# Optimization experiments

Hardware: AMD Instinct MI355X
Metric: run time of the kernel (lower is better)

Reference implementation:

```python
import jax, jax.numpy as jnp
import numpy as np

N = 50000   # nodes
E = 800000  # edges
D_FEAT = 128
D_HID = 128
D_EMB = 128


def _xavier(key, shape):
    fan_in, fan_out = shape
    lim = float(np.sqrt(6.0 / (fan_in + fan_out)))
    return jax.random.uniform(key, shape, jnp.float32, -lim, lim)


def setup_inputs() -> dict:
    key = jax.random.key(0)
    ks = jax.random.split(key, 12)
    return {
        "x": jax.random.normal(ks[0], (N, D_FEAT), jnp.float32),
        "edge_index": jax.random.randint(ks[1], (2, E), 0, N),
        "x_aug": jax.random.normal(ks[2], (N, D_FEAT), jnp.float32),
        "edge_index_aug": jax.random.randint(ks[3], (2, E), 0, N),
        # GCNConv weights (PyG stores lin.weight [out,in]; we use [in,out])
        "W_in": _xavier(ks[4], (D_FEAT, D_HID)),
        "b_in": jnp.zeros((D_HID,), jnp.float32),
        "W_h": _xavier(ks[5], (D_HID, D_HID)),
        "b_h": jnp.zeros((D_HID,), jnp.float32),
        "W_out": _xavier(ks[6], (D_HID, D_EMB)),
        "b_out": jnp.zeros((D_EMB,), jnp.float32),
        # fc head: Linear(embed,hidden) -> ReLU -> Linear(hidden,embed)
        "Wf1": _xavier(ks[7], (D_EMB, D_HID)),
        "bf1": jnp.zeros((D_HID,), jnp.float32),
        "Wf2": _xavier(ks[8], (D_HID, D_EMB)),
        "bf2": jnp.zeros((D_EMB,), jnp.float32),
    }


def gcn_layer(x, W, b, src, dst):
    """GCNConv: out = D^{-1/2}(A+I)D^{-1/2} (x @ W) + b, deg counted with self-loops."""
    n = x.shape[0]
    h = x @ W                                    # [N, out]
    deg = jax.ops.segment_sum(jnp.ones(src.shape[0], x.dtype), dst, num_segments=n) + 1.0
    dis = jax.lax.rsqrt(deg)                      # deg >= 1 due to self-loop
    norm = dis[src] * dis[dst]                    # [E]
    agg = jax.ops.segment_sum(h[src] * norm[:, None], dst, num_segments=n)
    agg = agg + h * (dis * dis)[:, None]          # self-loop contribution
    return agg + b


def gcn_forward(x, edge_index, W_in, b_in, W_h, b_h, W_out, b_out, Wf1, bf1, Wf2, bf2):
    src, dst = edge_index[0], edge_index[1]
    x = jax.nn.relu(gcn_layer(x, W_in, b_in, src, dst))
    # dropout(p=0.5, training=False) is identity in eval mode
    x = jax.nn.relu(gcn_layer(x, W_h, b_h, src, dst))
    x = jax.nn.relu(gcn_layer(x, W_out, b_out, src, dst))
    x = jax.nn.relu(x @ Wf1 + bf1) @ Wf2 + bf2
    return x


def reference(x, edge_index, x_aug, edge_index_aug, W_in, b_in, W_h, b_h,
              W_out, b_out, Wf1, bf1, Wf2, bf2):
    out = gcn_forward(x, edge_index, W_in, b_in, W_h, b_h, W_out, b_out, Wf1, bf1, Wf2, bf2)
    out_aug = gcn_forward(x_aug, edge_index_aug, W_in, b_in, W_h, b_h, W_out, b_out, Wf1, bf1, Wf2, bf2)
    return (out, out_aug)
```

## Files before the change

kernel.cpp:

```cpp
#include <hip/hip_runtime.h>
#include <hip/hip_bf16.h>

#define D 128

typedef __bf16 bf16x8 __attribute__((ext_vector_type(8)));
typedef float  f32x4  __attribute__((ext_vector_type(4)));


__global__ void k_zero_i32(int* __restrict__ p, int n) {
    int i = blockIdx.x * blockDim.x + threadIdx.x;
    if (i < n) p[i] = 0;
}

__global__ void k_copy_i32(int* __restrict__ dst, const int* __restrict__ src, int n) {
    int i = blockIdx.x * blockDim.x + threadIdx.x;
    if (i < n) dst[i] = src[i];
}

__global__ void k_count_deg(const int* __restrict__ dst, int* __restrict__ deg, int e) {
    int i = blockIdx.x * blockDim.x + threadIdx.x;
    if (i < e) atomicAdd(&deg[dst[i]], 1);
}

__global__ void k_dis(const int* __restrict__ deg, float* __restrict__ dis, int n) {
    int i = blockIdx.x * blockDim.x + threadIdx.x;
    if (i < n) dis[i] = rsqrtf((float)deg[i] + 1.0f);
}


__global__ __launch_bounds__(256) void k_scan1(const int* __restrict__ deg,
                                               int* __restrict__ rowptr,
                                               int* __restrict__ bsum, int n) {
    __shared__ int tmp[256];
    int t = threadIdx.x;
    int i = blockIdx.x * 256 + t;
    tmp[t] = (i < n) ? deg[i] : 0;
    __syncthreads();
    for (int ofs = 1; ofs < 256; ofs <<= 1) {
        int add = (t >= ofs) ? tmp[t - ofs] : 0;
        __syncthreads();
        tmp[t] += add;
        __syncthreads();
    }
    if (i < n) rowptr[i + 1] = tmp[t];
    if (t == 255) bsum[blockIdx.x] = tmp[255];
}

__global__ __launch_bounds__(256) void k_scan2(int* __restrict__ bsum, int nb) {
    __shared__ int tmp[256];
    int t = threadIdx.x;
    tmp[t] = (t < nb) ? bsum[t] : 0;
    __syncthreads();
    for (int ofs = 1; ofs < 256; ofs <<= 1) {
        int add = (t >= ofs) ? tmp[t - ofs] : 0;
        __syncthreads();
        tmp[t] += add;
        __syncthreads();
    }
    if (t < nb) bsum[t] = tmp[t];
}

__global__ void k_scan3(int* __restrict__ rowptr, const int* __restrict__ bsum, int n) {
    int i = blockIdx.x * blockDim.x + threadIdx.x;
    if (i == 0) rowptr[0] = 0;
    if (i < n) {
        int b = i >> 8;
        if (b > 0) rowptr[i + 1] += bsum[b - 1];
    }
}

__global__ void k_csr_fill(const int* __restrict__ src, const int* __restrict__ dst,
                           int* __restrict__ cursor, int* __restrict__ csr_src, int e) {
    int i = blockIdx.x * blockDim.x + threadIdx.x;
    if (i < e) {
        int pos = atomicAdd(&cursor[dst[i]], 1);
        csr_src[pos] = src[i];
    }
}


__global__ __launch_bounds__(256) void k_pack_w5(
    const float* __restrict__ w0, const float* __restrict__ w1,
    const float* __restrict__ w2, const float* __restrict__ w3,
    const float* __restrict__ w4, __bf16* __restrict__ out) {
    int q = blockIdx.x >> 6;
    const float* W = (q == 0) ? w0 : (q == 1) ? w1 : (q == 2) ? w2 : (q == 3) ? w3 : w4;
    int i = ((blockIdx.x & 63) << 8) | threadIdx.x;
    int j    = i & 7;
    int lane = (i >> 3) & 63;
    int ct   = (i >> 9) & 7;
    int kb   = i >> 12;
    int k = kb * 32 + (lane >> 4) * 8 + j;
    int c = ct * 16 + (lane & 15);
    float w = W[k * D + c];
    __bf16 hi = (__bf16)w;
    __bf16 lo = (__bf16)(w - (float)hi);
    __bf16* dstp = out + (size_t)q * 32768;
    dstp[i] = hi;
    dstp[16384 + i] = lo;
}


__global__ __launch_bounds__(256) void k_gemm_mfma(
    const float* __restrict__ A, const __bf16* __restrict__ Wp,
    const float* __restrict__ bias, float* __restrict__ C, int n,
    int fuse_bias, int fuse_relu) {
    __shared__ __bf16 Ws[32768];
    int t = threadIdx.x;
    for (int i = t * 8; i < 32768; i += 2048)
        *(float4*)&Ws[i] = *(const float4*)&Wp[i];

    int wv = t >> 6, lane = t & 63;
    int lrow = lane & 15, lhi = lane >> 4;
    int m0 = blockIdx.x * 64 + wv * 16;

    bf16x8 ahi[4], alo[4];
    int arow = m0 + lrow;
    const float* ap = A + (size_t)arow * D + lhi * 8;
    #pragma unroll
    for (int kb = 0; kb < 4; ++kb) {
        float av[8];
        if (arow < n) {
            float4 p0 = *(const float4*)(ap + kb * 32);
            float4 p1 = *(const float4*)(ap + kb * 32 + 4);
            av[0] = p0.x; av[1] = p0.y; av[2] = p0.z; av[3] = p0.w;
            av[4] = p1.x; av[5] = p1.y; av[6] = p1.z; av[7] = p1.w;
        } else {
            #pragma unroll
            for (int j = 0; j < 8; ++j) av[j] = 0.0f;
        }
        #pragma unroll
        for (int j = 0; j < 8; ++j) {
            __bf16 h = (__bf16)av[j];
            ahi[kb][j] = h;
            alo[kb][j] = (__bf16)(av[j] - (float)h);
        }
    }
    __syncthreads();

    f32x4 acc[8];
    f32x4 zz = {0.f, 0.f, 0.f, 0.f};
    #pragma unroll
    for (int i = 0; i < 8; ++i) acc[i] = zz;

    #pragma unroll
    for (int kb = 0; kb < 4; ++kb) {
        #pragma unroll
        for (int ct = 0; ct < 8; ++ct) {
            int off = ((kb * 8 + ct) * 64 + lane) * 8;
            bf16x8 bh = *(const bf16x8*)&Ws[off];
            bf16x8 bl = *(const bf16x8*)&Ws[16384 + off];
            acc[ct] = __builtin_amdgcn_mfma_f32_16x16x32_bf16(ahi[kb], bh, acc[ct], 0, 0, 0);
            acc[ct] = __builtin_amdgcn_mfma_f32_16x16x32_bf16(ahi[kb], bl, acc[ct], 0, 0, 0);
            acc[ct] = __builtin_amdgcn_mfma_f32_16x16x32_bf16(alo[kb], bh, acc[ct], 0, 0, 0);
        }
    }

    #pragma unroll
    for (int ct = 0; ct < 8; ++ct) {
        int col = ct * 16 + lrow;
        float bv = fuse_bias ? bias[col] : 0.0f;
        #pragma unroll
        for (int r = 0; r < 4; ++r) {
            int row = m0 + lhi * 4 + r;
            if (row < n) {
                float v = acc[ct][r] + bv;
                if (fuse_relu) v = fmaxf(v, 0.0f);
                C[(size_t)row * D + col] = v;
            }
        }
    }
}


__global__ __launch_bounds__(256) void k_csr_agg(
    const float* __restrict__ H, const int* __restrict__ rowptr,
    const int* __restrict__ csr_src, const float* __restrict__ dis,
    const float* __restrict__ bias, float* __restrict__ X, int n, int relu) {
    int wid = (blockIdx.x * 256 + threadIdx.x) >> 6;
    int lane = threadIdx.x & 63;
    int v = __builtin_amdgcn_readfirstlane(wid);
    if (v >= n) return;
    float dv = dis[v];
    const float* Hv = H + (size_t)v * D;
    float acc0 = Hv[lane] * dv * dv;
    float acc1 = Hv[lane + 64] * dv * dv;
    int beg = rowptr[v], end = rowptr[v + 1];
    int j = beg;
    for (; j + 4 <= end; j += 4) {
        int s0 = csr_src[j + 0], s1 = csr_src[j + 1];
        int s2 = csr_src[j + 2], s3 = csr_src[j + 3];
        float w0 = dis[s0] * dv, w1 = dis[s1] * dv;
        float w2 = dis[s2] * dv, w3 = dis[s3] * dv;
        const float* p0 = H + (size_t)s0 * D;
        const float* p1 = H + (size_t)s1 * D;
        const float* p2 = H + (size_t)s2 * D;
        const float* p3 = H + (size_t)s3 * D;
        float a0 = p0[lane], b0 = p0[lane + 64];
        float a1 = p1[lane], b1 = p1[lane + 64];
        float a2 = p2[lane], b2 = p2[lane + 64];
        float a3 = p3[lane], b3 = p3[lane + 64];
        acc0 = fmaf(a0, w0, acc0); acc1 = fmaf(b0, w0, acc1);
        acc0 = fmaf(a1, w1, acc0); acc1 = fmaf(b1, w1, acc1);
        acc0 = fmaf(a2, w2, acc0); acc1 = fmaf(b2, w2, acc1);
        acc0 = fmaf(a3, w3, acc0); acc1 = fmaf(b3, w3, acc1);
    }
    for (; j < end; ++j) {
        int s = csr_src[j];
        float w = dis[s] * dv;
        const float* p = H + (size_t)s * D;
        acc0 = fmaf(p[lane], w, acc0);
        acc1 = fmaf(p[lane + 64], w, acc1);
    }
    acc0 += bias[lane];
    acc1 += bias[lane + 64];
    if (relu) { acc0 = fmaxf(acc0, 0.f); acc1 = fmaxf(acc1, 0.f); }
    X[(size_t)v * D + lane] = acc0;
    X[(size_t)v * D + lane + 64] = acc1;
}


extern "C" void kernel_launch(void* const* d_in, const int* in_sizes, int n_in,
                              void* d_out, int out_size, void* d_ws, size_t ws_size,
                              hipStream_t stream) {
    const float* x    = (const float*)d_in[0];
    const int*   ei   = (const int*)d_in[1];
    const float* xa   = (const float*)d_in[2];
    const int*   eia  = (const int*)d_in[3];
    const float* W_in = (const float*)d_in[4];
    const float* b_in = (const float*)d_in[5];
    const float* W_h  = (const float*)d_in[6];
    const float* b_h  = (const float*)d_in[7];
    const float* W_out= (const float*)d_in[8];
    const float* b_out= (const float*)d_in[9];
    const float* Wf1  = (const float*)d_in[10];
    const float* bf1  = (const float*)d_in[11];
    const float* Wf2  = (const float*)d_in[12];
    const float* bf2  = (const float*)d_in[13];

    const int n = in_sizes[0] / D;
    const int e = in_sizes[1] / 2;

    float* Xf     = (float*)d_ws;
    float* H      = Xf + (size_t)n * D;
    float* dis    = H  + (size_t)n * D;
    int*   deg    = (int*)(dis + n);
    int*   rowptr = deg + n;
    int*   cursor = rowptr + (n + 4);
    int*   bsum   = cursor + n;
    int*   csrsrc = bsum + 256;
    __bf16* wpack = (__bf16*)(csrsrc + e);

    float* out = (float*)d_out;

    const float* bl[3] = {b_in, b_h, b_out};

    const int threads = 256;
    const int g_n    = (n + threads - 1) / threads;
    const int g_e    = (e + threads - 1) / threads;
    const int g_gemm = (n + 63) / 64;
    const int g_agg  = (n * 64 + threads - 1) / threads;

    k_pack_w5<<<320, threads, 0, stream>>>(W_in, W_h, W_out, Wf1, Wf2, wpack);

    for (int g = 0; g < 2; ++g) {
        const float* xin = g ? xa : x;
        const int* src  = g ? eia : ei;
        const int* dst  = src + e;
        float* outg = out + (size_t)g * n * D;

        k_zero_i32<<<g_n, threads, 0, stream>>>(deg, n);
        k_count_deg<<<g_e, threads, 0, stream>>>(dst, deg, e);
        k_dis<<<g_n, threads, 0, stream>>>(deg, dis, n);
        k_scan1<<<g_n, threads, 0, stream>>>(deg, rowptr, bsum, n);
        k_scan2<<<1, threads, 0, stream>>>(bsum, g_n);
        k_scan3<<<g_n, threads, 0, stream>>>(rowptr, bsum, n);
        k_copy_i32<<<g_n, threads, 0, stream>>>(cursor, rowptr, n);
        k_csr_fill<<<g_e, threads, 0, stream>>>(src, dst, cursor, csrsrc, e);

        for (int l = 0; l < 3; ++l) {
            const float* Ain = (l == 0) ? xin : Xf;
            k_gemm_mfma<<<g_gemm, threads, 0, stream>>>(Ain, wpack + (size_t)l * 32768,
                                                        nullptr, H, n, 0, 0);
            k_csr_agg<<<g_agg, threads, 0, stream>>>(H, rowptr, csrsrc, dis, bl[l], Xf, n, 1);
        }

        k_gemm_mfma<<<g_gemm, threads, 0, stream>>>(Xf, wpack + (size_t)3 * 32768,
                                                    bf1, H, n, 1, 1);
        k_gemm_mfma<<<g_gemm, threads, 0, stream>>>(H, wpack + (size_t)4 * 32768,
                                                    bf2, outg, n, 1, 0);
    }
}
```

Baseline: 921.7 us.

## Build both graphs' CSR in one pass and split aggregation across two waves

Combines the degree count, prefix scan and CSR fill for the original and augmented graphs into single launches over concatenated node and edge ranges, with the augmented graph's node ids offset by n0. The scan now carries totals across more than 256 blocks and writes the cursor copy directly, so the zero and copy kernels go away. Aggregation now assigns each node to two wavefronts, each handling 64 channels, with 8 neighbours unrolled per step to give more parallelism and more loads in flight. The cost is that each neighbour's index and dis value are loaded by both wavefronts.

```diff
diff --git a/kernel.cpp b/kernel.cpp
--- a/kernel.cpp
+++ b/kernel.cpp
@@ -7,26 +7,17 @@
 typedef float  f32x4  __attribute__((ext_vector_type(4)));
 
 
-__global__ void k_zero_i32(int* __restrict__ p, int n) {
-    int i = blockIdx.x * blockDim.x + threadIdx.x;
-    if (i < n) p[i] = 0;
-}
-
-__global__ void k_copy_i32(int* __restrict__ dst, const int* __restrict__ src, int n) {
-    int i = blockIdx.x * blockDim.x + threadIdx.x;
-    if (i < n) dst[i] = src[i];
-}
-
-__global__ void k_count_deg(const int* __restrict__ dst, int* __restrict__ deg, int e) {
-    int i = blockIdx.x * blockDim.x + threadIdx.x;
-    if (i < e) atomicAdd(&deg[dst[i]], 1);
+__global__ void k_count_deg2(const int* __restrict__ ei, const int* __restrict__ eia,
+                             int* __restrict__ deg, int e0, int e1, int n0) {
+    int i = blockIdx.x * blockDim.x + threadIdx.x;
+    if (i < e0) atomicAdd(&deg[ei[e0 + i]], 1);
+    else if (i < e0 + e1) { int k = i - e0; atomicAdd(&deg[eia[e1 + k] + n0], 1); }
 }
 
 __global__ void k_dis(const int* __restrict__ deg, float* __restrict__ dis, int n) {
     int i = blockIdx.x * blockDim.x + threadIdx.x;
     if (i < n) dis[i] = rsqrtf((float)deg[i] + 1.0f);
 }
-
 
 __global__ __launch_bounds__(256) void k_scan1(const int* __restrict__ deg,
                                                int* __restrict__ rowptr,
@@ -49,33 +40,47 @@
 __global__ __launch_bounds__(256) void k_scan2(int* __restrict__ bsum, int nb) {
     __shared__ int tmp[256];
     int t = threadIdx.x;
-    tmp[t] = (t < nb) ? bsum[t] : 0;
-    __syncthreads();
-    for (int ofs = 1; ofs < 256; ofs <<= 1) {
-        int add = (t >= ofs) ? tmp[t - ofs] : 0;
-        __syncthreads();
-        tmp[t] += add;
-        __syncthreads();
-    }
-    if (t < nb) bsum[t] = tmp[t];
-}
-
-__global__ void k_scan3(int* __restrict__ rowptr, const int* __restrict__ bsum, int n) {
-    int i = blockIdx.x * blockDim.x + threadIdx.x;
-    if (i == 0) rowptr[0] = 0;
+    int carry = 0;
+    for (int base = 0; base < nb; base += 256) {
+        int idx = base + t;
+        tmp[t] = (idx < nb) ? bsum[idx] : 0;
+        __syncthreads();
+        for (int ofs = 1; ofs < 256; ofs <<= 1) {
+            int add = (t >= ofs) ? tmp[t - ofs] : 0;
+            __syncthreads();
+            tmp[t] += add;
+            __syncthreads();
+        }
+        if (idx < nb) bsum[idx] = tmp[t] + carry;
+        int total = tmp[255];
+        __syncthreads();
+        carry += total;
+    }
+}
+
+__global__ void k_scan3(int* __restrict__ rowptr, int* __restrict__ cursor,
+                        const int* __restrict__ bsum, int n) {
+    int i = blockIdx.x * blockDim.x + threadIdx.x;
+    if (i == 0) { rowptr[0] = 0; cursor[0] = 0; }
     if (i < n) {
         int b = i >> 8;
-        if (b > 0) rowptr[i + 1] += bsum[b - 1];
-    }
-}
-
-__global__ void k_csr_fill(const int* __restrict__ src, const int* __restrict__ dst,
-                           int* __restrict__ cursor, int* __restrict__ csr_src, int e) {
-    int i = blockIdx.x * blockDim.x + threadIdx.x;
-    if (i < e) {
-        int pos = atomicAdd(&cursor[dst[i]], 1);
-        csr_src[pos] = src[i];
-    }
+        int val = rowptr[i + 1];
+        if (b > 0) val += bsum[b - 1];
+        rowptr[i + 1] = val;
+        if (i + 1 < n) cursor[i + 1] = val;
+    }
+}
+
+__global__ void k_csr_fill2(const int* __restrict__ ei, const int* __restrict__ eia,
+                            int* __restrict__ cursor, int* __restrict__ csr_src,
+                            int e0, int e1, int n0) {
+    int i = blockIdx.x * blockDim.x + threadIdx.x;
+    int s, d;
+    if (i < e0) { s = ei[i]; d = ei[e0 + i]; }
+    else if (i < e0 + e1) { int k = i - e0; s = eia[k]; d = eia[e1 + k] + n0; }
+    else return;
+    int pos = atomicAdd(&cursor[d], 1);
+    csr_src[pos] = s;
 }
 
 
@@ -173,50 +178,39 @@
 }
 
 
-__global__ __launch_bounds__(256) void k_csr_agg(
+__global__ __launch_bounds__(256) void k_csr_agg2(
     const float* __restrict__ H, const int* __restrict__ rowptr,
     const int* __restrict__ csr_src, const float* __restrict__ dis,
     const float* __restrict__ bias, float* __restrict__ X, int n, int relu) {
     int wid = (blockIdx.x * 256 + threadIdx.x) >> 6;
     int lane = threadIdx.x & 63;
-    int v = __builtin_amdgcn_readfirstlane(wid);
+    int w = __builtin_amdgcn_readfirstlane(wid);
+    int v = w >> 1;
+    int half = w & 1;
     if (v >= n) return;
+    int ch = half * 64 + lane;
     float dv = dis[v];
-    const float* Hv = H + (size_t)v * D;
-    float acc0 = Hv[lane] * dv * dv;
-    float acc1 = Hv[lane + 64] * dv * dv;
+    float acc = H[(size_t)v * D + ch] * dv * dv;
     int beg = rowptr[v], end = rowptr[v + 1];
     int j = beg;
-    for (; j + 4 <= end; j += 4) {
-        int s0 = csr_src[j + 0], s1 = csr_src[j + 1];
-        int s2 = csr_src[j + 2], s3 = csr_src[j + 3];
-        float w0 = dis[s0] * dv, w1 = dis[s1] * dv;
-        float w2 = dis[s2] * dv, w3 = dis[s3] * dv;
-        const float* p0 = H + (size_t)s0 * D;
-        const float* p1 = H + (size_t)s1 * D;
-        const float* p2 = H + (size_t)s2 * D;
-        const float* p3 = H + (size_t)s3 * D;
-        float a0 = p0[lane], b0 = p0[lane + 64];
-        float a1 = p1[lane], b1 = p1[lane + 64];
-        float a2 = p2[lane], b2 = p2[lane + 64];
-        float a3 = p3[lane], b3 = p3[lane + 64];
-        acc0 = fmaf(a0, w0, acc0); acc1 = fmaf(b0, w0, acc1);
-        acc0 = fmaf(a1, w1, acc0); acc1 = fmaf(b1, w1, acc1);
-        acc0 = fmaf(a2, w2, acc0); acc1 = fmaf(b2, w2, acc1);
-        acc0 = fmaf(a3, w3, acc0); acc1 = fmaf(b3, w3, acc1);
+    for (; j + 8 <= end; j += 8) {
+        int s[8]; float ww[8]; float a[8];
+        #pragma unroll
+        for (int q = 0; q < 8; ++q) s[q] = csr_src[j + q];
+        #pragma unroll
+        for (int q = 0; q < 8; ++q) ww[q] = dis[s[q]] * dv;
+        #pragma unroll
+        for (int q = 0; q < 8; ++q) a[q] = H[(size_t)s[q] * D + ch];
+        #pragma unroll
+        for (int q = 0; q < 8; ++q) acc = fmaf(a[q], ww[q], acc);
     }
     for (; j < end; ++j) {
         int s = csr_src[j];
-        float w = dis[s] * dv;
-        const float* p = H + (size_t)s * D;
-        acc0 = fmaf(p[lane], w, acc0);
-        acc1 = fmaf(p[lane + 64], w, acc1);
-    }
-    acc0 += bias[lane];
-    acc1 += bias[lane + 64];
-    if (relu) { acc0 = fmaxf(acc0, 0.f); acc1 = fmaxf(acc1, 0.f); }
-    X[(size_t)v * D + lane] = acc0;
-    X[(size_t)v * D + lane + 64] = acc1;
+        acc = fmaf(H[(size_t)s * D + ch], dis[s] * dv, acc);
+    }
+    acc += bias[ch];
+    if (relu) acc = fmaxf(acc, 0.f);
+    X[(size_t)v * D + ch] = acc;
 }
 
 
@@ -238,56 +232,60 @@
     const float* Wf2  = (const float*)d_in[12];
     const float* bf2  = (const float*)d_in[13];
 
-    const int n = in_sizes[0] / D;
-    const int e = in_sizes[1] / 2;
+    const int n0 = in_sizes[0] / D;
+    const int e0 = in_sizes[1] / 2;
+    const int n1 = in_sizes[2] / D;
+    const int e1 = in_sizes[3] / 2;
+    const int nt = n0 + n1;
+    const int et = e0 + e1;
 
     float* Xf     = (float*)d_ws;
-    float* H      = Xf + (size_t)n * D;
-    float* dis    = H  + (size_t)n * D;
-    int*   deg    = (int*)(dis + n);
-    int*   rowptr = deg + n;
-    int*   cursor = rowptr + (n + 4);
-    int*   bsum   = cursor + n;
-    int*   csrsrc = bsum + 256;
-    __bf16* wpack = (__bf16*)(csrsrc + e);
+    float* H      = Xf + (size_t)n0 * D;
+    float* dis    = H  + (size_t)n0 * D;
+    int*   deg    = (int*)(dis + nt);
+    int*   rowptr = deg + nt;
+    int*   cursor = rowptr + (nt + 4);
+    int*   bsum   = cursor + nt;
+    int*   csrsrc = bsum + 512;
+    __bf16* wpack = (__bf16*)(csrsrc + et);
 
     float* out = (float*)d_out;
 
     const float* bl[3] = {b_in, b_h, b_out};
 
     const int threads = 256;
-    const int g_n    = (n + threads - 1) / threads;
-    const int g_e    = (e + threads - 1) / threads;
-    const int g_gemm = (n + 63) / 64;
-    const int g_agg  = (n * 64 + threads - 1) / threads;
+    const int g_nt   = (nt + threads - 1) / threads;
+    const int g_et   = (et + threads - 1) / threads;
+    const int g_gemm = (n0 + 63) / 64;
+    const int g_agg  = (n0 * 2 * 64 + threads - 1) / threads;
+    const int nb     = g_nt;
 
     k_pack_w5<<<320, threads, 0, stream>>>(W_in, W_h, W_out, Wf1, Wf2, wpack);
 
+    hipMemsetAsync(deg, 0, (size_t)nt * sizeof(int), stream);
+    k_count_deg2<<<g_et, threads, 0, stream>>>(ei, eia, deg, e0, e1, n0);
+    k_dis<<<g_nt, threads, 0, stream>>>(deg, dis, nt);
+    k_scan1<<<g_nt, threads, 0, stream>>>(deg, rowptr, bsum, nt);
+    k_scan2<<<1, threads, 0, stream>>>(bsum, nb);
+    k_scan3<<<g_nt, threads, 0, stream>>>(rowptr, cursor, bsum, nt);
+    k_csr_fill2<<<g_et, threads, 0, stream>>>(ei, eia, cursor, csrsrc, e0, e1, n0);
+
     for (int g = 0; g < 2; ++g) {
-        const float* xin = g ? xa : x;
-        const int* src  = g ? eia : ei;
-        const int* dst  = src + e;
-        float* outg = out + (size_t)g * n * D;
-
-        k_zero_i32<<<g_n, threads, 0, stream>>>(deg, n);
-        k_count_deg<<<g_e, threads, 0, stream>>>(dst, deg, e);
-        k_dis<<<g_n, threads, 0, stream>>>(deg, dis, n);
-        k_scan1<<<g_n, threads, 0, stream>>>(deg, rowptr, bsum, n);
-        k_scan2<<<1, threads, 0, stream>>>(bsum, g_n);
-        k_scan3<<<g_n, threads, 0, stream>>>(rowptr, bsum, n);
-        k_copy_i32<<<g_n, threads, 0, stream>>>(cursor, rowptr, n);
-        k_csr_fill<<<g_e, threads, 0, stream>>>(src, dst, cursor, csrsrc, e);
+        const float* xin   = g ? xa : x;
+        const int*   rpg   = rowptr + (size_t)g * n0;
+        const float* disg  = dis + (size_t)g * n0;
+        float* outg = out + (size_t)g * n0 * D;
 
         for (int l = 0; l < 3; ++l) {
             const float* Ain = (l == 0) ? xin : Xf;
             k_gemm_mfma<<<g_gemm, threads, 0, stream>>>(Ain, wpack + (size_t)l * 32768,
-                                                        nullptr, H, n, 0, 0);
-            k_csr_agg<<<g_agg, threads, 0, stream>>>(H, rowptr, csrsrc, dis, bl[l], Xf, n, 1);
+                                                        nullptr, H, n0, 0, 0);
+            k_csr_agg2<<<g_agg, threads, 0, stream>>>(H, rpg, csrsrc, disg, bl[l], Xf, n0, 1);
         }
 
         k_gemm_mfma<<<g_gemm, threads, 0, stream>>>(Xf, wpack + (size_t)3 * 32768,
-                                                    bf1, H, n, 1, 1);
+                                                    bf1, H, n0, 1, 1);
         k_gemm_mfma<<<g_gemm, threads, 0, stream>>>(H, wpack + (size_t)4 * 32768,
-                                                    bf2, outg, n, 1, 0);
-    }
-}
+                                                    bf2, outg, n0, 1, 0);
+    }
+}
```

New measurement: 960.8 us. 4.2% more time.
